# Optimization experiments

Hardware: AMD Instinct MI355X
Metric: run time of the kernel (lower is better)

## Reference

```python
import jax, jax.numpy as jnp
import numpy as np

T, B, D = 512, 32, 1024

def setup_inputs() -> dict:
    key = jax.random.key(0)
    ks = jax.random.split(key, 4)
    scale = 1.0 / np.sqrt(D)
    x = jax.random.normal(ks[0], (T, B, D), dtype=jnp.float32)
    h0 = jnp.zeros((B, D), dtype=jnp.float32)
    W_alpha = jax.random.normal(ks[1], (D, D), dtype=jnp.float32) * scale
    b_alpha = jnp.zeros((D,), dtype=jnp.float32)
    # W_h in torch is orthogonal * 0.3; approximate with scaled gaussian of matching norm
    W_h = jax.random.normal(ks[2], (D, D), dtype=jnp.float32) * (0.3 * scale)
    W_x = jax.random.normal(ks[3], (D, D), dtype=jnp.float32) * scale
    b = jnp.zeros((D,), dtype=jnp.float32)
    return {"x": x, "h0": h0, "W_alpha": W_alpha, "b_alpha": b_alpha,
            "W_h": W_h, "W_x": W_x, "b": b}

def reference(x, h0, W_alpha, b_alpha, W_h, W_x, b):
    # Precompute input-dependent projections for all timesteps (batched GEMM)
    alpha_x_all = jnp.einsum('tbd,ed->tbe', x, W_alpha) + b_alpha  # [T,B,D]
    Wx_all = jnp.einsum('tbd,ed->tbe', x, W_x)                     # [T,B,D]

    def step(h_prev, inp):
        alpha_x_t, wx_t = inp
        alpha = jax.nn.sigmoid(alpha_x_t)
        v = jnp.tanh(h_prev @ W_h.T + wx_t + b)
        h_new = h_prev + alpha * v  # residual: identity path always present
        return h_new, h_new

    _, h_seq = jax.lax.scan(step, h0, (alpha_x_all, Wx_all))  # [T,B,D]
    h = jnp.concatenate([h0[None], h_seq], axis=0)            # [T+1,B,D]
    output = h_seq * jax.nn.silu(h_seq)                       # h * silu(h)
    return output, h
```

## Files before the change

### kernel.cpp

```cpp
#include <hip/hip_runtime.h>

typedef __bf16 bf16x8 __attribute__((ext_vector_type(8)));
typedef float  f32x4  __attribute__((ext_vector_type(4)));
typedef unsigned short u16;
typedef unsigned int   u32;
typedef unsigned long long u64;
typedef u16 u16x8 __attribute__((ext_vector_type(8)));

#define TT 512
#define BB 32
#define DD 1024

#define WS_Z   0
#define WS_HX  134217728
#define WS_FLG (134217728+262144)

static __device__ __forceinline__ u16 f2b(float f){
  u32 u = __builtin_bit_cast(u32, f);
  u32 r = (u + 0x7fffu + ((u>>16)&1u)) >> 16;
  return (u16)r;
}
static __device__ __forceinline__ float b2f(u16 h){
  return __builtin_bit_cast(float, (u32)h<<16);
}

#define AL32(p)   __hip_atomic_load((p),      __ATOMIC_RELAXED, __HIP_MEMORY_SCOPE_AGENT)
#define AL64(p)   __hip_atomic_load((p),      __ATOMIC_RELAXED, __HIP_MEMORY_SCOPE_AGENT)
#define AS32(p,v) __hip_atomic_store((p),(v), __ATOMIC_RELAXED, __HIP_MEMORY_SCOPE_AGENT)

#define MFMA16(a,b,c) __builtin_amdgcn_mfma_f32_16x16x32_bf16(a,b,c,0,0,0)

__global__ __launch_bounds__(256) void k_gemm3(const float* __restrict__ X,
    const float* __restrict__ Wa, const float* __restrict__ Wx,
    float* __restrict__ Z){
  __shared__ u16 Ahi[128*64];
  __shared__ u16 Alo[128*64];
  __shared__ u16 Bhi[128*64];
  __shared__ u16 Blo[128*64];
  int id  = blockIdx.x;
  int swz = (id & 7)*256 + (id>>3);
  int mblk = swz>>4, nblk = swz&15;
  const float* W = (nblk < 8) ? Wa : Wx;
  int n0 = (nblk&7)*128;
  int m0 = mblk*128;
  int tid = threadIdx.x, lane = tid&63, w = tid>>6;
  int wm = w>>1, wn = w&1;
  int sr = tid>>1, sh = tid&1;

  f32x4 acc[4][4];
  #pragma unroll
  for (int i=0;i<4;i++)
    #pragma unroll
    for (int j=0;j<4;j++) acc[i][j] = (f32x4){0.f,0.f,0.f,0.f};

  for (int kb = 0; kb < DD; kb += 64){
    const float* sa  = X + (size_t)(m0+sr)*DD + kb + sh*32;
    const float* sbp = W + (size_t)(n0+sr)*DD + kb + sh*32;
    int rswz = (sr&7)<<4;
    #pragma unroll
    for (int g=0; g<4; g++){
      float4 va0 = ((const float4*)sa)[g*2];
      float4 va1 = ((const float4*)sa)[g*2+1];
      float4 vb0 = ((const float4*)sbp)[g*2];
      float4 vb1 = ((const float4*)sbp)[g*2+1];
      float fa[8] = {va0.x,va0.y,va0.z,va0.w,va1.x,va1.y,va1.z,va1.w};
      float fb[8] = {vb0.x,vb0.y,vb0.z,vb0.w,vb1.x,vb1.y,vb1.z,vb1.w};
      u16x8 ah, al, bh, bl;
      #pragma unroll
      for (int j=0;j<8;j++){
        u16 ha = f2b(fa[j]); ah[j] = ha; al[j] = f2b(fa[j] - b2f(ha));
        u16 hb = f2b(fb[j]); bh[j] = hb; bl[j] = f2b(fb[j] - b2f(hb));
      }
      int off = sr*128 + ((sh*64 + g*16) ^ rswz);
      *(u16x8*)((char*)Ahi + off) = ah;
      *(u16x8*)((char*)Alo + off) = al;
      *(u16x8*)((char*)Bhi + off) = bh;
      *(u16x8*)((char*)Blo + off) = bl;
    }
    __syncthreads();
    #pragma unroll
    for (int ks=0; ks<2; ks++){
      int kby = ks*64 + ((lane>>4)<<4);
      bf16x8 ahf[4], alf[4], bhf[4], blf[4];
      #pragma unroll
      for (int mi=0;mi<4;mi++){
        int row = wm*64 + mi*16 + (lane&15);
        int ao = row*128 + (kby ^ ((row&7)<<4));
        ahf[mi] = *(const bf16x8*)((const char*)Ahi + ao);
        alf[mi] = *(const bf16x8*)((const char*)Alo + ao);
      }
      #pragma unroll
      for (int ni=0;ni<4;ni++){
        int row = wn*64 + ni*16 + (lane&15);
        int bo = row*128 + (kby ^ ((row&7)<<4));
        bhf[ni] = *(const bf16x8*)((const char*)Bhi + bo);
        blf[ni] = *(const bf16x8*)((const char*)Blo + bo);
      }
      #pragma unroll
      for (int mi=0;mi<4;mi++)
        #pragma unroll
        for (int ni=0;ni<4;ni++){
          acc[mi][ni] = MFMA16(ahf[mi], bhf[ni], acc[mi][ni]);
          acc[mi][ni] = MFMA16(ahf[mi], blf[ni], acc[mi][ni]);
          acc[mi][ni] = MFMA16(alf[mi], bhf[ni], acc[mi][ni]);
        }
    }
    __syncthreads();
  }

  #pragma unroll
  for (int mi=0;mi<4;mi++){
    #pragma unroll
    for (int ni=0;ni<4;ni++){
      int colz = nblk*128 + wn*64 + ni*16 + (lane&15);
      #pragma unroll
      for (int q=0;q<4;q++){
        int rowm = m0 + wm*64 + mi*16 + ((lane>>4)<<2) + q;
        Z[(size_t)rowm*2048 + colz] = acc[mi][ni][q];
      }
    }
  }
}

__global__ void k_init(const float* __restrict__ h0, float* __restrict__ hout0,
                       u32* __restrict__ hx, u32* __restrict__ flg){
  int i = blockIdx.x*blockDim.x + threadIdx.x;
  if (i < BB*DD){
    float v = h0[i];
    hout0[i] = v;
    u16 hh = f2b(v);
    u16 ll = f2b(v - b2f(hh));
    hx[i] = (u32)hh | ((u32)ll<<16);
  }
  if (i < 32) flg[i] = 0u;
  if (i == 32) flg[1024] = 0u;
}

#define UNPK(c, A, B) do { \
  u16x8 hi8, lo8; \
  hi8[0]=(u16)A.x; lo8[0]=(u16)(A.x>>16); \
  hi8[1]=(u16)A.y; lo8[1]=(u16)(A.y>>16); \
  hi8[2]=(u16)A.z; lo8[2]=(u16)(A.z>>16); \
  hi8[3]=(u16)A.w; lo8[3]=(u16)(A.w>>16); \
  hi8[4]=(u16)B.x; lo8[4]=(u16)(B.x>>16); \
  hi8[5]=(u16)B.y; lo8[5]=(u16)(B.y>>16); \
  hi8[6]=(u16)B.z; lo8[6]=(u16)(B.z>>16); \
  hi8[7]=(u16)B.w; lo8[7]=(u16)(B.w>>16); \
  int off_ = srow*2048 + ((kseg*128 + (c)*16) ^ ssw); \
  *(u16x8*)((char*)Hhi + off_) = hi8; \
  *(u16x8*)((char*)Hlo + off_) = lo8; \
} while(0)

__global__ __launch_bounds__(512, 2) void k_recur9(
    const float* __restrict__ Z, const float* __restrict__ Wh,
    const float* __restrict__ h0,
    const float* __restrict__ balpha, const float* __restrict__ bvec,
    float* __restrict__ out0,
    float* __restrict__ hout,
    u32* __restrict__ hx,
    u32* __restrict__ flg){
  __shared__ u16 Hhi[BB*DD];
  __shared__ u16 Hlo[BB*DD];
  __shared__ f32x4 Red[4][64];
  __shared__ int sdone;

  int blk = blockIdx.x;
  int tid = threadIdx.x, lane = tid&63, w = tid>>6;

  if (blk >= 32){
    if (tid == 0) sdone = 0;
    __syncthreads();
    float a = (float)tid + 1.0f;
    float m = 1.000001f, c = 0.9999991f;
    for (;;){
      for (int i = 0; i < 512; i++){
        asm volatile("v_fmac_f32 %0, %1, %2" : "+v"(a) : "v"(m), "v"(c));
      }
      if (tid == 0) sdone = (int)AL32(flg + 1024);
      __syncthreads();
      if (sdone) break;
      __syncthreads();
    }
    asm volatile("" :: "v"(a));
    return;
  }

  int e0 = blk*32;
  int kh = w>>2, wm = (w>>1)&1, wn = w&1;

  bf16x8 wfh[16], wfl[16];
  {
    const float* wrow = Wh + (size_t)(e0 + wn*16 + (lane&15))*DD
                           + kh*512 + ((lane>>4)<<3);
    #pragma unroll
    for (int ks=0; ks<16; ks++){
      float4 a = ((const float4*)(wrow + ks*32))[0];
      float4 b = ((const float4*)(wrow + ks*32))[1];
      float f[8] = {a.x,a.y,a.z,a.w,b.x,b.y,b.z,b.w};
      u16x8 uh, ul;
      #pragma unroll
      for (int j=0;j<8;j++){
        u16 hh = f2b(f[j]);
        uh[j] = hh;
        ul[j] = f2b(f[j] - b2f(hh));
      }
      wfh[ks] = __builtin_bit_cast(bf16x8, uh);
      wfl[ks] = __builtin_bit_cast(bf16x8, ul);
    }
  }

  int el = e0 + wn*16 + (lane&15);
  float ba = balpha[el], bb = bvec[el];
  float hc[4]  = {0.f,0.f,0.f,0.f};
  float ov[4]  = {0.f,0.f,0.f,0.f};
  float axr[4] = {0.f,0.f,0.f,0.f};
  float wxr[4] = {0.f,0.f,0.f,0.f};
  if (kh == 0){
    #pragma unroll
    for (int q=0;q<4;q++){
      int b = wm*16 + ((lane>>4)<<2) + q;
      hc[q]  = h0[b*DD + el];
      axr[q] = Z[(size_t)b*2048 + el];
      wxr[q] = Z[(size_t)b*2048 + DD + el];
    }
  }

  int srow = tid & 31;
  int kseg = tid >> 5;
  int ssw  = (srow & 15) << 4;

  for (int t=0;t<TT;t++){
    if (tid < 16){
      const u64* fp = (const u64*)(flg + tid*2);
      u64 fl = AL64(fp);
      while ((u32)fl < (u32)t || (u32)(fl>>32) < (u32)t) fl = AL64(fp);
    }
    __syncthreads();

    const u32* hsrc = hx + (size_t)(t&1)*BB*DD;
    const void* gp = (const void*)(hsrc + srow*DD + kseg*64);
    uint4 r0,r1,r2,r3,r4,r5,r6,r7,r8,r9,rA,rB,rC,rD,rE,rF;
    asm volatile(
      "global_load_dwordx4 %0, %16, off sc1\n\t"
      "global_load_dwordx4 %1, %16, off offset:16 sc1\n\t"
      "global_load_dwordx4 %2, %16, off offset:32 sc1\n\t"
      "global_load_dwordx4 %3, %16, off offset:48 sc1\n\t"
      "global_load_dwordx4 %4, %16, off offset:64 sc1\n\t"
      "global_load_dwordx4 %5, %16, off offset:80 sc1\n\t"
      "global_load_dwordx4 %6, %16, off offset:96 sc1\n\t"
      "global_load_dwordx4 %7, %16, off offset:112 sc1\n\t"
      "global_load_dwordx4 %8, %16, off offset:128 sc1\n\t"
      "global_load_dwordx4 %9, %16, off offset:144 sc1\n\t"
      "global_load_dwordx4 %10, %16, off offset:160 sc1\n\t"
      "global_load_dwordx4 %11, %16, off offset:176 sc1\n\t"
      "global_load_dwordx4 %12, %16, off offset:192 sc1\n\t"
      "global_load_dwordx4 %13, %16, off offset:208 sc1\n\t"
      "global_load_dwordx4 %14, %16, off offset:224 sc1\n\t"
      "global_load_dwordx4 %15, %16, off offset:240 sc1\n\t"
      "s_waitcnt vmcnt(0)"
      : "=&v"(r0), "=&v"(r1), "=&v"(r2), "=&v"(r3),
        "=&v"(r4), "=&v"(r5), "=&v"(r6), "=&v"(r7),
        "=&v"(r8), "=&v"(r9), "=&v"(rA), "=&v"(rB),
        "=&v"(rC), "=&v"(rD), "=&v"(rE), "=&v"(rF)
      : "v"(gp)
      : "memory");
    UNPK(0, r0, r1);  UNPK(1, r2, r3);
    UNPK(2, r4, r5);  UNPK(3, r6, r7);
    UNPK(4, r8, r9);  UNPK(5, rA, rB);
    UNPK(6, rC, rD);  UNPK(7, rE, rF);

    float axc[4], wxc[4];
    if (kh == 0){
      #pragma unroll
      for (int q=0;q<4;q++){ axc[q]=axr[q]; wxc[q]=wxr[q]; }
      if (t < TT-1){
        #pragma unroll
        for (int q=0;q<4;q++){
          int b = wm*16 + ((lane>>4)<<2) + q;
          size_t zi = ((size_t)(t+1)*BB + b)*2048 + el;
          axr[q] = Z[zi]; wxr[q] = Z[zi + DD];
        }
      }
    } else {
      #pragma unroll
      for (int q=0;q<4;q++){ axc[q]=0.f; wxc[q]=0.f; }
    }
    __syncthreads();

    f32x4 a0 = (f32x4){0.f,0.f,0.f,0.f};
    f32x4 a1 = (f32x4){0.f,0.f,0.f,0.f};
    f32x4 a2 = (f32x4){0.f,0.f,0.f,0.f};
    int ra    = wm*16 + (lane&15);
    int rbase = ra*2048;
    int rsw   = (ra&15)<<4;
    int kb0   = kh*1024 + ((lane>>4)<<4);
    #pragma unroll
    for (int ks=0; ks<16; ks++){
      int off = rbase + ((kb0 + ks*64) ^ rsw);
      bf16x8 ahi = *(const bf16x8*)((const char*)Hhi + off);
      bf16x8 alo = *(const bf16x8*)((const char*)Hlo + off);
      a0 = MFMA16(ahi, wfh[ks], a0);
      a1 = MFMA16(ahi, wfl[ks], a1);
      a2 = MFMA16(alo, wfh[ks], a2);
    }
    f32x4 acc = a0 + a1 + a2;
    if (kh == 1){ Red[wm*2+wn][lane] = acc; }
    __syncthreads();

    if (kh == 0){
      acc += Red[wm*2+wn][lane];
      u32* hnx = hx + (size_t)((t+1)&1)*BB*DD;
      #pragma unroll
      for (int q=0;q<4;q++){
        int b = wm*16 + ((lane>>4)<<2) + q;
        float ax = axc[q] + ba;
        float alpha = 1.f/(1.f + __expf(-ax));
        float s  = acc[q] + wxc[q] + bb;
        float as = fabsf(s);
        float e2 = __expf(-2.f*as);
        float vv = __builtin_copysignf((1.f - e2)/(1.f + e2), s);
        float h = hc[q] + alpha*vv;
        hc[q] = h;
        float sg = 1.f/(1.f + __expf(-h));
        ov[q] = h*h*sg;
        u16 hh = f2b(h);
        u16 ll = f2b(h - b2f(hh));
        AS32(hnx + b*DD + el, (u32)hh | ((u32)ll<<16));
      }
    }

    __syncthreads();
    if (tid == 0) AS32(flg + blk, (u32)(t+1));

    if (kh == 0){
      #pragma unroll
      for (int q=0;q<4;q++){
        int b = wm*16 + ((lane>>4)<<2) + q;
        size_t oi = (size_t)t*(BB*DD) + (size_t)b*DD + el;
        out0[oi] = ov[q];
        hout[oi + BB*DD] = hc[q];
      }
    }
  }

  if (tid == 0) AS32(flg + 1024, 1u);
}

extern "C" void kernel_launch(void* const* d_in, const int* in_sizes, int n_in,
                              void* d_out, int out_size, void* d_ws, size_t ws_size,
                              hipStream_t stream){
  (void)in_sizes; (void)n_in; (void)out_size; (void)ws_size;
  const float* x   = (const float*)d_in[0];
  const float* h0  = (const float*)d_in[1];
  const float* Wa  = (const float*)d_in[2];
  const float* bal = (const float*)d_in[3];
  const float* Whf = (const float*)d_in[4];
  const float* Wxf = (const float*)d_in[5];
  const float* bv  = (const float*)d_in[6];

  char* ws = (char*)d_ws;
  float* Zb  = (float*)(ws + WS_Z);
  u32*   hx  = (u32*)(ws + WS_HX);
  u32*   flg = (u32*)(ws + WS_FLG);

  float* out0 = (float*)d_out;
  float* hout = (float*)d_out + (size_t)TT*BB*DD;

  k_gemm3<<<2048, 256, 0, stream>>>(x, Wa, Wxf, Zb);
  k_init<<<(BB*DD+255)/256, 256, 0, stream>>>(h0, hout, hx, flg);

  void* args[] = {(void*)&Zb, (void*)&Whf, (void*)&h0, (void*)&bal, (void*)&bv,
                  (void*)&out0, (void*)&hout, (void*)&hx, (void*)&flg};
  hipLaunchCooperativeKernel((const void*)k_recur9, dim3(256), dim3(512),
                             args, 0, stream);
}
```

Baseline: 4.600 ms.

## Replace per-step block barrier with LDS counter publish and defer output stores

Removes the end-of-step __syncthreads before the flag publish. The four kh==0 waves now wait for their h stores to drain and bump a shared counter, and wave 4 spins on that counter before writing the block's progress flag. The out0/hout stores for step t-1 move into the next step and are issued alongside the h-burst loads, so their latency overlaps the load wait; the last step's outputs are written after the loop. This shortens the critical path of the cross-block recurrence handoff, at the cost of a spin-waiting wave and extra ordering subtleties around vmcnt.

```diff
diff --git a/kernel.cpp b/kernel.cpp
--- a/kernel.cpp
+++ b/kernel.cpp
@@ -10,10 +10,11 @@
 #define TT 512
 #define BB 32
 #define DD 1024
+#define BBDD (BB*DD)
 
 #define WS_Z   0
 #define WS_HX  134217728
-#define WS_FLG (134217728+262144)
+#define WS_FLG 134479872
 
 static __device__ __forceinline__ u16 f2b(float f){
   u32 u = __builtin_bit_cast(u32, f);
@@ -151,7 +152,32 @@
   *(u16x8*)((char*)Hlo + off_) = lo8; \
 } while(0)
 
-__global__ __launch_bounds__(512, 2) void k_recur9(
+#define BURST16_ISSUE(GP) \
+    asm volatile( \
+      "global_load_dwordx4 %0, %16, off sc1\n\t" \
+      "global_load_dwordx4 %1, %16, off offset:16 sc1\n\t" \
+      "global_load_dwordx4 %2, %16, off offset:32 sc1\n\t" \
+      "global_load_dwordx4 %3, %16, off offset:48 sc1\n\t" \
+      "global_load_dwordx4 %4, %16, off offset:64 sc1\n\t" \
+      "global_load_dwordx4 %5, %16, off offset:80 sc1\n\t" \
+      "global_load_dwordx4 %6, %16, off offset:96 sc1\n\t" \
+      "global_load_dwordx4 %7, %16, off offset:112 sc1\n\t" \
+      "global_load_dwordx4 %8, %16, off offset:128 sc1\n\t" \
+      "global_load_dwordx4 %9, %16, off offset:144 sc1\n\t" \
+      "global_load_dwordx4 %10, %16, off offset:160 sc1\n\t" \
+      "global_load_dwordx4 %11, %16, off offset:176 sc1\n\t" \
+      "global_load_dwordx4 %12, %16, off offset:192 sc1\n\t" \
+      "global_load_dwordx4 %13, %16, off offset:208 sc1\n\t" \
+      "global_load_dwordx4 %14, %16, off offset:224 sc1\n\t" \
+      "global_load_dwordx4 %15, %16, off offset:240 sc1" \
+      : "=&v"(r0), "=&v"(r1), "=&v"(r2), "=&v"(r3), \
+        "=&v"(r4), "=&v"(r5), "=&v"(r6), "=&v"(r7), \
+        "=&v"(r8), "=&v"(r9), "=&v"(rA), "=&v"(rB), \
+        "=&v"(rC), "=&v"(rD), "=&v"(rE), "=&v"(rF) \
+      : "v"(GP) \
+      : "memory")
+
+__global__ __launch_bounds__(512, 2) void k_recur16(
     const float* __restrict__ Z, const float* __restrict__ Wh,
     const float* __restrict__ h0,
     const float* __restrict__ balpha, const float* __restrict__ bvec,
@@ -162,6 +188,7 @@
   __shared__ u16 Hhi[BB*DD];
   __shared__ u16 Hlo[BB*DD];
   __shared__ f32x4 Red[4][64];
+  __shared__ u32 PubCnt;
   __shared__ int sdone;
 
   int blk = blockIdx.x;
@@ -187,6 +214,8 @@
 
   int e0 = blk*32;
   int kh = w>>2, wm = (w>>1)&1, wn = w&1;
+
+  if (tid == 0) PubCnt = 0;
 
   bf16x8 wfh[16], wfl[16];
   {
@@ -228,6 +257,7 @@
   int srow = tid & 31;
   int kseg = tid >> 5;
   int ssw  = (srow & 15) << 4;
+  __syncthreads();
 
   for (int t=0;t<TT;t++){
     if (tid < 16){
@@ -237,33 +267,26 @@
     }
     __syncthreads();
 
-    const u32* hsrc = hx + (size_t)(t&1)*BB*DD;
+    const u32* hsrc = hx + (size_t)(t&1)*BBDD;
     const void* gp = (const void*)(hsrc + srow*DD + kseg*64);
     uint4 r0,r1,r2,r3,r4,r5,r6,r7,r8,r9,rA,rB,rC,rD,rE,rF;
-    asm volatile(
-      "global_load_dwordx4 %0, %16, off sc1\n\t"
-      "global_load_dwordx4 %1, %16, off offset:16 sc1\n\t"
-      "global_load_dwordx4 %2, %16, off offset:32 sc1\n\t"
-      "global_load_dwordx4 %3, %16, off offset:48 sc1\n\t"
-      "global_load_dwordx4 %4, %16, off offset:64 sc1\n\t"
-      "global_load_dwordx4 %5, %16, off offset:80 sc1\n\t"
-      "global_load_dwordx4 %6, %16, off offset:96 sc1\n\t"
-      "global_load_dwordx4 %7, %16, off offset:112 sc1\n\t"
-      "global_load_dwordx4 %8, %16, off offset:128 sc1\n\t"
-      "global_load_dwordx4 %9, %16, off offset:144 sc1\n\t"
-      "global_load_dwordx4 %10, %16, off offset:160 sc1\n\t"
-      "global_load_dwordx4 %11, %16, off offset:176 sc1\n\t"
-      "global_load_dwordx4 %12, %16, off offset:192 sc1\n\t"
-      "global_load_dwordx4 %13, %16, off offset:208 sc1\n\t"
-      "global_load_dwordx4 %14, %16, off offset:224 sc1\n\t"
-      "global_load_dwordx4 %15, %16, off offset:240 sc1\n\t"
-      "s_waitcnt vmcnt(0)"
-      : "=&v"(r0), "=&v"(r1), "=&v"(r2), "=&v"(r3),
-        "=&v"(r4), "=&v"(r5), "=&v"(r6), "=&v"(r7),
-        "=&v"(r8), "=&v"(r9), "=&v"(rA), "=&v"(rB),
-        "=&v"(rC), "=&v"(rD), "=&v"(rE), "=&v"(rF)
-      : "v"(gp)
-      : "memory");
+    BURST16_ISSUE(gp);
+    if (kh == 0){
+      int tp = (t > 0) ? (t-1) : 0;
+      float* o0 = out0 + (size_t)tp*BBDD;
+      float* h1 = hout + (size_t)tp*BBDD + BBDD;
+      #pragma unroll
+      for (int q=0;q<4;q++){
+        int b = wm*16 + ((lane>>4)<<2) + q;
+        o0[b*DD + el] = ov[q];
+        h1[b*DD + el] = hc[q];
+      }
+      asm volatile("s_waitcnt vmcnt(8)" ::: "memory");
+    } else {
+      asm volatile("s_waitcnt vmcnt(0)" ::: "memory");
+    }
+    __builtin_amdgcn_sched_barrier(0);
+
     UNPK(0, r0, r1);  UNPK(1, r2, r3);
     UNPK(2, r4, r5);  UNPK(3, r6, r7);
     UNPK(4, r8, r9);  UNPK(5, rA, rB);
@@ -309,7 +332,7 @@
 
     if (kh == 0){
       acc += Red[wm*2+wn][lane];
-      u32* hnx = hx + (size_t)((t+1)&1)*BB*DD;
+      u32* hnx = hx + (size_t)((t+1)&1)*BBDD;
       #pragma unroll
       for (int q=0;q<4;q++){
         int b = wm*16 + ((lane>>4)<<2) + q;
@@ -327,22 +350,25 @@
         u16 ll = f2b(h - b2f(hh));
         AS32(hnx + b*DD + el, (u32)hh | ((u32)ll<<16));
       }
-    }
-
-    __syncthreads();
-    if (tid == 0) AS32(flg + blk, (u32)(t+1));
-
-    if (kh == 0){
-      #pragma unroll
-      for (int q=0;q<4;q++){
-        int b = wm*16 + ((lane>>4)<<2) + q;
-        size_t oi = (size_t)t*(BB*DD) + (size_t)b*DD + el;
-        out0[oi] = ov[q];
-        hout[oi + BB*DD] = hc[q];
-      }
-    }
-  }
-
+      asm volatile("s_waitcnt vmcnt(0)" ::: "memory");
+      if (lane == 0) atomicAdd(&PubCnt, 1u);
+    } else if (w == 4){
+      volatile u32* pc = &PubCnt;
+      u32 tgt = 4u*(u32)(t+1);
+      while (*pc < tgt) {}
+      if (lane == 0) AS32(flg + blk, (u32)(t+1));
+    }
+  }
+
+  if (kh == 0){
+    #pragma unroll
+    for (int q=0;q<4;q++){
+      int b = wm*16 + ((lane>>4)<<2) + q;
+      size_t oi = (size_t)(TT-1)*BBDD + (size_t)b*DD + el;
+      out0[oi] = ov[q];
+      hout[oi + BBDD] = hc[q];
+    }
+  }
   if (tid == 0) AS32(flg + 1024, 1u);
 }
 
@@ -371,6 +397,6 @@
 
   void* args[] = {(void*)&Zb, (void*)&Whf, (void*)&h0, (void*)&bal, (void*)&bv,
                   (void*)&out0, (void*)&hout, (void*)&hx, (void*)&flg};
-  hipLaunchCooperativeKernel((const void*)k_recur9, dim3(256), dim3(512),
+  hipLaunchCooperativeKernel((const void*)k_recur16, dim3(256), dim3(512),
                              args, 0, stream);
 }
```

New measurement: 5.296 ms. 1.15x slower.
